# Kernel tuning notes

Hardware: AMD Instinct MI355X
Metric: run time of the kernel (lower is better)

The kernel has to match this reference:

```python
import jax, jax.numpy as jnp
import numpy as np

B, G, IN, F, O = 65536, 6, 512, 256, 18


def setup_inputs() -> dict:
    key = jax.random.key(0)
    ks = jax.random.split(key, 9)
    return {
        "state": jax.random.normal(ks[0], (B, IN), dtype=jnp.float32),
        "action": jax.random.randint(ks[1], (B, 1), 0, O, dtype=jnp.int64),
        "idx": jax.random.randint(ks[2], (B,), 0, G, dtype=jnp.int64),
        # per-game expert Linear weights (stored [in, out] so fwd is x @ W)
        "W1": jax.random.normal(ks[3], (G, IN, F), dtype=jnp.float32) * (1.0 / np.sqrt(IN)),
        "b1": jnp.zeros((G, F), dtype=jnp.float32),
        # shared layer
        "W2": jax.random.normal(ks[4], (F, F), dtype=jnp.float32) * (1.0 / np.sqrt(F)),
        "b2": jnp.zeros((F,), dtype=jnp.float32),
        # per-game Q heads
        "Wq": jax.random.normal(ks[5], (G, F, O), dtype=jnp.float32) * (1.0 / np.sqrt(F)),
        "bq": jnp.zeros((G, O), dtype=jnp.float32),
    }


def reference(state, action, idx, W1, b1, W2, b2, Wq, bq):
    # The torch code processes samples grouped by np.unique(idx) and then
    # torch.cat's the groups: this is a stable sort of samples by idx value.
    perm = jnp.argsort(idx)  # jnp.argsort is stable by default
    sp = state[perm]         # [B, IN], samples in group-sorted order
    ip = idx[perm]           # [B]

    # per-game expert: compute all G tiny linears, select the routed one
    h_all = jax.nn.sigmoid(jnp.einsum('bi,gif->bgf', sp, W1) + b1)  # [B,G,F]
    h1 = jnp.take_along_axis(h_all, ip[:, None, None], axis=1)[:, 0, :]  # [B,F]

    # shared layer ('relu' branch)
    h_f = jax.nn.relu(h1 @ W2 + b2)  # [B,F]

    # stacked per-game heads
    q = jnp.tanh(jnp.einsum('bf,gfo->bgo', h_f, Wq) + bq)  # [B,G,O]

    # action gather: q_acted[b,g] = q[b,g,action[b,0]] (action in ORIGINAL order,
    # exactly as in the torch code, which gathers on the permuted-row q)
    a = jnp.broadcast_to(action[:, :1], (B, G))[..., None]  # [B,G,1]
    q_acted = jnp.take_along_axis(q, a, axis=2)[..., 0]     # [B,G]

    # idx gather (again with idx in ORIGINAL order, matching the torch code)
    q_out = jnp.take_along_axis(q_acted, idx[:, None], axis=1)[:, 0]  # [B]
    return q_out
```

## Files before the change

kernel.cpp:

```cpp
#include <hip/hip_runtime.h>
#include <hip/hip_bf16.h>
#include <math.h>

#define B_N 65536
#define G_N 6
#define IN_N 512
#define F_N 256
#define O_N 18

#define NB 256
#define CHUNK 256

#define TBM 32
#define MAXT (B_N / TBM + G_N)

typedef __bf16 bf16x8 __attribute__((ext_vector_type(8)));
typedef float f32x4 __attribute__((ext_vector_type(4)));

#define WS_BC     0
#define WS_BOFF   8192
#define WS_NTILES 16448
#define WS_DESC   16512
#define WS_W1F    65536
#define WS_W2F    (WS_W1F + 1572864)
#define WS_WQT    (WS_W2F + 131072)
#define WS_PERM   4194304

__device__ __forceinline__ unsigned packcvt(float a, float b) {
    __hip_bfloat162 h = __float22bfloat162_rn(float2{a, b});
    union { __hip_bfloat162 h; unsigned u; } c; c.h = h; return c.u;
}
__device__ __forceinline__ unsigned short f2bf(float f) {
    union { float f; unsigned u; } a; a.f = f;
    unsigned r = a.u + 0x7fffu + ((a.u >> 16) & 1u);
    return (unsigned short)(r >> 16);
}
__device__ __forceinline__ bf16x8 asbf(uint4 u) {
    union { uint4 u; bf16x8 b; } c; c.u = u; return c.b;
}
__device__ __forceinline__ float fast_tanh(float x) {
    float e = __expf(2.0f * x);
    return 1.0f - 2.0f / (e + 1.0f);
}

__global__ void k_hist(const int* __restrict__ idx, int* __restrict__ bc) {
    __shared__ int cnt[G_N];
    int t = threadIdx.x;
    if (t < G_N) cnt[t] = 0;
    __syncthreads();
    int e = blockIdx.x * CHUNK + t;
    atomicAdd(&cnt[idx[e]], 1);
    __syncthreads();
    if (t < G_N) bc[blockIdx.x * G_N + t] = cnt[t];
}

__global__ void k_prefix(const int* __restrict__ bc, int* __restrict__ boff,
                         int* __restrict__ ntiles, int* __restrict__ desc) {
    __shared__ int sbc[NB * G_N];
    __shared__ int tot[G_N], st[G_N];
    __shared__ int tstart[G_N + 1];
    int t = threadIdx.x;
    for (int i = t; i < NB * G_N; i += 256) sbc[i] = bc[i];
    __syncthreads();
    int w = t >> 6, l = t & 63;
    for (int g = w; g < G_N; g += 4) {
        int v[4]; int s = 0;
#pragma unroll
        for (int j = 0; j < 4; j++) { v[j] = sbc[(l * 4 + j) * G_N + g]; s += v[j]; }
        int inc = s;
#pragma unroll
        for (int o = 1; o < 64; o <<= 1) { int x = __shfl_up(inc, o, 64); if (l >= o) inc += x; }
        int run = inc - s;
        if (l == 63) tot[g] = inc;
#pragma unroll
        for (int j = 0; j < 4; j++) { sbc[(l * 4 + j) * G_N + g] = run; run += v[j]; }
    }
    __syncthreads();
    if (t == 0) {
        int acc = 0;
        for (int g = 0; g < G_N; g++) { st[g] = acc; acc += tot[g]; }
        int nt = 0;
        for (int g = 0; g < G_N; g++) { tstart[g] = nt; nt += (tot[g] + TBM - 1) / TBM; }
        tstart[G_N] = nt;
        *ntiles = nt;
    }
    __syncthreads();
    for (int i = t; i < NB * G_N; i += 256) boff[i] = sbc[i] + st[i % G_N];
    int nt = tstart[G_N];
    for (int i = t; i < MAXT; i += 256) {
        int gd = 0, r0 = 0, nr = 0;
        if (i < nt) {
            int g = 0;
            while (g < G_N - 1 && i >= tstart[g + 1]) g++;
            int k = i - tstart[g];
            r0 = st[g] + k * TBM;
            int rem = tot[g] - k * TBM;
            nr = rem < TBM ? rem : TBM;
            gd = g;
        }
        desc[i * 3 + 0] = gd; desc[i * 3 + 1] = r0; desc[i * 3 + 2] = nr;
    }
}

__global__ void k_scatter(const int* __restrict__ idx, const int* __restrict__ boff,
                          int* __restrict__ perm) {
    __shared__ int wcnt[4][G_N];
    __shared__ int base[G_N];
    int t = threadIdx.x, w = t >> 6, l = t & 63;
    int e = blockIdx.x * CHUNK + t;
    int g = idx[e];
    int rank = 0;
    for (int gg = 0; gg < G_N; gg++) {
        unsigned long long m = __ballot(g == gg);
        if (g == gg) rank = __popcll(m & ((1ull << l) - 1ull));
        if (l == 0) wcnt[w][gg] = __popcll(m);
    }
    if (t < G_N) base[t] = boff[blockIdx.x * G_N + t];
    __syncthreads();
    int off = base[g] + rank;
    for (int ww = 0; ww < w; ww++) off += wcnt[ww][g];
    perm[off] = e;
}

__global__ void k_pack_all(const float* __restrict__ W1, const float* __restrict__ W2,
                           const float* __restrict__ Wq,
                           unsigned short* __restrict__ W1f, unsigned short* __restrict__ W2f,
                           float* __restrict__ WqT) {
    int kf = blockIdx.x, w = blockIdx.y, z = blockIdx.z;
    if (z == 6 && kf >= 8) {
        int tid = ((kf - 8) * 8 + w) * 128 + threadIdx.x;
        for (int e = tid; e < G_N * O_N * F_N; e += 8192) {
            int f = e & (F_N - 1);
            int go = e >> 8;
            int g = go / O_N, o = go - g * O_N;
            WqT[e] = Wq[((long)g * F_N + f) * O_N + o];
        }
        return;
    }
    const float* src;
    unsigned short* dst;
    int kfTot;
    if (z < 6) { src = W1 + (long)z * IN_N * F_N; dst = W1f + (long)z * IN_N * F_N; kfTot = 16; }
    else       { src = W2; dst = W2f; kfTot = 8; }
    int f = threadIdx.x >> 6, l = threadIdx.x & 63;
    int lrow = l & 15, q = l >> 4;
    int n = w * 32 + f * 16 + lrow;
    int k0 = kf * 32 + q * 8;
    const float* s = src + (long)k0 * F_N + n;
    unsigned o[4];
#pragma unroll
    for (int j = 0; j < 4; j++)
        o[j] = packcvt(s[(2 * j) * F_N], s[(2 * j + 1) * F_N]);
    unsigned short* d = dst + ((((long)w * kfTot + kf) * 2 + f) * 64 + l) * 8;
    uint4 v = { o[0], o[1], o[2], o[3] };
    *(uint4*)d = v;
}

__global__ __launch_bounds__(512, 6) void k_fused(
    const float* __restrict__ state, const char* __restrict__ w1f,
    const char* __restrict__ w2f, const float* __restrict__ wqt,
    const float* __restrict__ b1, const float* __restrict__ b2,
    const float* __restrict__ bqv,
    const int* __restrict__ action, const int* __restrict__ idx,
    const int* __restrict__ perm, const int* __restrict__ desc,
    float* __restrict__ out) {
    int td = blockIdx.x;
    int g = desc[td * 3 + 0], row0 = desc[td * 3 + 1], nr = desc[td * 3 + 2];
    if (nr == 0) return;

    __shared__ __align__(16) unsigned short smA[TBM * 512];
    __shared__ __align__(16) unsigned short smH[TBM * 256];
    __shared__ float partial[TBM][9];
    __shared__ int gq[TBM], actv[TBM];

    int t = threadIdx.x, w = t >> 6, l = t & 63;
    int lrow = l & 15, q = l >> 4;
    int x0 = lrow & 7;

    const char* B1 = w1f + (((long)g * 8 + w) << 15) + l * 16;
    uint4 nb0 = *(const uint4*)(B1);
    uint4 nb1 = *(const uint4*)(B1 + 1024);

    if (t < TBM) {
        int pos = row0 + t; if (pos > B_N - 1) pos = B_N - 1;
        gq[t] = idx[pos];
        actv[t] = action[pos];
    }

    {
        int m = t >> 4, s = t & 15;
        int pr = row0 + m; if (pr > B_N - 1) pr = B_N - 1;
        const float* src = state + (long)perm[pr] * IN_N + s * 4;
        int cb = s >> 1, h = s & 1, mx = m & 7;
        char* rowbase = (char*)smA + m * 1024 + h * 8;
#pragma unroll
        for (int j = 0; j < 8; j++) {
            float4 v = *(const float4*)(src + j * 64);
            uint2 p = { packcvt(v.x, v.y), packcvt(v.z, v.w) };
            int c = (cb + j * 8) ^ mx;
            *(uint2*)(rowbase + c * 16) = p;
        }
    }
    __syncthreads();

    const char* ar[2];
#pragma unroll
    for (int i = 0; i < 2; i++) ar[i] = (const char*)smA + (i * 16 + lrow) * 1024;

    f32x4 acc[2][2];
#pragma unroll
    for (int i = 0; i < 2; i++)
#pragma unroll
        for (int j = 0; j < 2; j++) acc[i][j] = (f32x4){0.f, 0.f, 0.f, 0.f};

#pragma unroll
    for (int kf = 0; kf < 16; kf++) {
        uint4 cb0 = nb0, cb1 = nb1;
        if (kf < 15) {
            nb0 = *(const uint4*)(B1 + (kf + 1) * 2048);
            nb1 = *(const uint4*)(B1 + (kf + 1) * 2048 + 1024);
        }
        int c = ((kf * 4 + q) ^ x0) * 16;
        bf16x8 af[2];
#pragma unroll
        for (int i = 0; i < 2; i++) af[i] = *(const bf16x8*)(ar[i] + c);
        bf16x8 b0 = asbf(cb0), b1v = asbf(cb1);
#pragma unroll
        for (int i = 0; i < 2; i++) {
            acc[i][0] = __builtin_amdgcn_mfma_f32_16x16x32_bf16(af[i], b0, acc[i][0], 0, 0, 0);
            acc[i][1] = __builtin_amdgcn_mfma_f32_16x16x32_bf16(af[i], b1v, acc[i][1], 0, 0, 0);
        }
    }

    const char* B2 = w2f + ((long)w << 14) + l * 16;
    uint4 m0 = *(const uint4*)(B2);
    uint4 m1 = *(const uint4*)(B2 + 1024);

    {
        int col0 = w * 32 + lrow;
        float bias0 = b1[g * F_N + col0];
        float bias1 = b1[g * F_N + col0 + 16];
        int cc = col0 >> 3, cb2 = (col0 & 7) * 2;
#pragma unroll
        for (int i = 0; i < 2; i++)
#pragma unroll
            for (int r = 0; r < 4; r++) {
                int row = i * 16 + q * 4 + r;
                float v0 = acc[i][0][r] + bias0;
                float v1 = acc[i][1][r] + bias1;
                float sg0 = 1.0f / (1.0f + __expf(-v0));
                float sg1 = 1.0f / (1.0f + __expf(-v1));
                unsigned pk = packcvt(sg0, sg1);
                int rx = row & 7;
                char* base = (char*)smH + row * 512 + cb2;
                *(unsigned short*)(base + ((cc)     ^ rx) * 16) = (unsigned short)pk;
                *(unsigned short*)(base + ((cc + 2) ^ rx) * 16) = (unsigned short)(pk >> 16);
            }
    }
    __syncthreads();

    const char* hr[2];
#pragma unroll
    for (int i = 0; i < 2; i++) hr[i] = (const char*)smH + (i * 16 + lrow) * 512;

    f32x4 acc2[2][2];
#pragma unroll
    for (int i = 0; i < 2; i++)
#pragma unroll
        for (int j = 0; j < 2; j++) acc2[i][j] = (f32x4){0.f, 0.f, 0.f, 0.f};

#pragma unroll
    for (int kf = 0; kf < 8; kf++) {
        uint4 c0 = m0, c1 = m1;
        if (kf < 7) {
            m0 = *(const uint4*)(B2 + (kf + 1) * 2048);
            m1 = *(const uint4*)(B2 + (kf + 1) * 2048 + 1024);
        }
        int c = ((kf * 4 + q) ^ x0) * 16;
        bf16x8 af[2];
#pragma unroll
        for (int i = 0; i < 2; i++) af[i] = *(const bf16x8*)(hr[i] + c);
        bf16x8 b0 = asbf(c0), b1v = asbf(c1);
#pragma unroll
        for (int i = 0; i < 2; i++) {
            acc2[i][0] = __builtin_amdgcn_mfma_f32_16x16x32_bf16(af[i], b0, acc2[i][0], 0, 0, 0);
            acc2[i][1] = __builtin_amdgcn_mfma_f32_16x16x32_bf16(af[i], b1v, acc2[i][1], 0, 0, 0);
        }
    }

    {
        int col0 = w * 32 + lrow;
        float bias0 = b2[col0], bias1 = b2[col0 + 16];
#pragma unroll
        for (int i = 0; i < 2; i++)
#pragma unroll
            for (int r = 0; r < 4; r++) {
                int row = i * 16 + q * 4 + r;
                const float* wp = wqt + ((long)gq[row] * O_N + actv[row]) * F_N;
                float v0 = fmaxf(acc2[i][0][r] + bias0, 0.0f);
                float v1 = fmaxf(acc2[i][1][r] + bias1, 0.0f);
                float s2 = v0 * wp[col0] + v1 * wp[col0 + 16];
                s2 += __shfl_xor(s2, 1, 64);
                s2 += __shfl_xor(s2, 2, 64);
                s2 += __shfl_xor(s2, 4, 64);
                s2 += __shfl_xor(s2, 8, 64);
                if (lrow == 0) partial[row][w] = s2;
            }
    }
    __syncthreads();
    if (t < TBM && t < nr) {
        float s2 = 0.f;
#pragma unroll
        for (int ww = 0; ww < 8; ww++) s2 += partial[t][ww];
        out[row0 + t] = fast_tanh(s2 + bqv[gq[t] * O_N + actv[t]]);
    }
}

extern "C" void kernel_launch(void* const* d_in, const int* in_sizes, int n_in,
                              void* d_out, int out_size, void* d_ws, size_t ws_size,
                              hipStream_t stream) {
    const float* state  = (const float*)d_in[0];
    const int*   action = (const int*)d_in[1];
    const int*   idx    = (const int*)d_in[2];
    const float* W1     = (const float*)d_in[3];
    const float* b1     = (const float*)d_in[4];
    const float* W2     = (const float*)d_in[5];
    const float* b2     = (const float*)d_in[6];
    const float* Wq     = (const float*)d_in[7];
    const float* bq     = (const float*)d_in[8];
    float* out = (float*)d_out;

    char* ws = (char*)d_ws;
    int* bc      = (int*)(ws + WS_BC);
    int* boff    = (int*)(ws + WS_BOFF);
    int* ntiles  = (int*)(ws + WS_NTILES);
    int* desc    = (int*)(ws + WS_DESC);
    unsigned short* W1f = (unsigned short*)(ws + WS_W1F);
    unsigned short* W2f = (unsigned short*)(ws + WS_W2F);
    float* WqT   = (float*)(ws + WS_WQT);
    int* perm    = (int*)(ws + WS_PERM);

    k_hist<<<NB, CHUNK, 0, stream>>>(idx, bc);
    k_prefix<<<1, 256, 0, stream>>>(bc, boff, ntiles, desc);
    k_scatter<<<NB, CHUNK, 0, stream>>>(idx, boff, perm);
    k_pack_all<<<dim3(16, 8, 7), 128, 0, stream>>>(W1, W2, Wq, W1f, W2f, WqT);
    k_fused<<<MAXT, 512, 0, stream>>>(state, (const char*)W1f, (const char*)W2f, WqT,
                                      b1, b2, bq, action, idx, perm, desc, out);
}
```

Measured before the change: 253.4 us.

## Merge all stages into one cooperative persistent kernel with grid syncs

Replaces the five separate launches (histogram, prefix, scatter, weight pack, fused MLP) with a single cooperative kernel that separates the phases with grid.sync(). The main MLP phase becomes a persistent loop over tile descriptors. The aim is to remove per-launch overhead and the inter-kernel gaps. In exchange it adds three grid-wide barriers, runs the prefix scan on one block while the rest wait, and caps the grid at 768 blocks, which may limit how the compute tiles are spread.

```diff
diff --git a/kernel.cpp b/kernel.cpp
--- a/kernel.cpp
+++ b/kernel.cpp
@@ -1,6 +1,9 @@
 #include <hip/hip_runtime.h>
 #include <hip/hip_bf16.h>
+#include <hip/hip_cooperative_groups.h>
 #include <math.h>
+
+namespace cg = cooperative_groups;
 
 #define B_N 65536
 #define G_N 6
@@ -19,7 +22,6 @@
 
 #define WS_BC     0
 #define WS_BOFF   8192
-#define WS_NTILES 16448
 #define WS_DESC   16512
 #define WS_W1F    65536
 #define WS_W2F    (WS_W1F + 1572864)
@@ -30,11 +32,6 @@
     __hip_bfloat162 h = __float22bfloat162_rn(float2{a, b});
     union { __hip_bfloat162 h; unsigned u; } c; c.h = h; return c.u;
 }
-__device__ __forceinline__ unsigned short f2bf(float f) {
-    union { float f; unsigned u; } a; a.f = f;
-    unsigned r = a.u + 0x7fffu + ((a.u >> 16) & 1u);
-    return (unsigned short)(r >> 16);
-}
 __device__ __forceinline__ bf16x8 asbf(uint4 u) {
     union { uint4 u; bf16x8 b; } c; c.u = u; return c.b;
 }
@@ -43,92 +40,12 @@
     return 1.0f - 2.0f / (e + 1.0f);
 }
 
-__global__ void k_hist(const int* __restrict__ idx, int* __restrict__ bc) {
-    __shared__ int cnt[G_N];
-    int t = threadIdx.x;
-    if (t < G_N) cnt[t] = 0;
-    __syncthreads();
-    int e = blockIdx.x * CHUNK + t;
-    atomicAdd(&cnt[idx[e]], 1);
-    __syncthreads();
-    if (t < G_N) bc[blockIdx.x * G_N + t] = cnt[t];
-}
-
-__global__ void k_prefix(const int* __restrict__ bc, int* __restrict__ boff,
-                         int* __restrict__ ntiles, int* __restrict__ desc) {
-    __shared__ int sbc[NB * G_N];
-    __shared__ int tot[G_N], st[G_N];
-    __shared__ int tstart[G_N + 1];
-    int t = threadIdx.x;
-    for (int i = t; i < NB * G_N; i += 256) sbc[i] = bc[i];
-    __syncthreads();
-    int w = t >> 6, l = t & 63;
-    for (int g = w; g < G_N; g += 4) {
-        int v[4]; int s = 0;
-#pragma unroll
-        for (int j = 0; j < 4; j++) { v[j] = sbc[(l * 4 + j) * G_N + g]; s += v[j]; }
-        int inc = s;
-#pragma unroll
-        for (int o = 1; o < 64; o <<= 1) { int x = __shfl_up(inc, o, 64); if (l >= o) inc += x; }
-        int run = inc - s;
-        if (l == 63) tot[g] = inc;
-#pragma unroll
-        for (int j = 0; j < 4; j++) { sbc[(l * 4 + j) * G_N + g] = run; run += v[j]; }
-    }
-    __syncthreads();
-    if (t == 0) {
-        int acc = 0;
-        for (int g = 0; g < G_N; g++) { st[g] = acc; acc += tot[g]; }
-        int nt = 0;
-        for (int g = 0; g < G_N; g++) { tstart[g] = nt; nt += (tot[g] + TBM - 1) / TBM; }
-        tstart[G_N] = nt;
-        *ntiles = nt;
-    }
-    __syncthreads();
-    for (int i = t; i < NB * G_N; i += 256) boff[i] = sbc[i] + st[i % G_N];
-    int nt = tstart[G_N];
-    for (int i = t; i < MAXT; i += 256) {
-        int gd = 0, r0 = 0, nr = 0;
-        if (i < nt) {
-            int g = 0;
-            while (g < G_N - 1 && i >= tstart[g + 1]) g++;
-            int k = i - tstart[g];
-            r0 = st[g] + k * TBM;
-            int rem = tot[g] - k * TBM;
-            nr = rem < TBM ? rem : TBM;
-            gd = g;
-        }
-        desc[i * 3 + 0] = gd; desc[i * 3 + 1] = r0; desc[i * 3 + 2] = nr;
-    }
-}
-
-__global__ void k_scatter(const int* __restrict__ idx, const int* __restrict__ boff,
-                          int* __restrict__ perm) {
-    __shared__ int wcnt[4][G_N];
-    __shared__ int base[G_N];
-    int t = threadIdx.x, w = t >> 6, l = t & 63;
-    int e = blockIdx.x * CHUNK + t;
-    int g = idx[e];
-    int rank = 0;
-    for (int gg = 0; gg < G_N; gg++) {
-        unsigned long long m = __ballot(g == gg);
-        if (g == gg) rank = __popcll(m & ((1ull << l) - 1ull));
-        if (l == 0) wcnt[w][gg] = __popcll(m);
-    }
-    if (t < G_N) base[t] = boff[blockIdx.x * G_N + t];
-    __syncthreads();
-    int off = base[g] + rank;
-    for (int ww = 0; ww < w; ww++) off += wcnt[ww][g];
-    perm[off] = e;
-}
-
-__global__ void k_pack_all(const float* __restrict__ W1, const float* __restrict__ W2,
-                           const float* __restrict__ Wq,
-                           unsigned short* __restrict__ W1f, unsigned short* __restrict__ W2f,
-                           float* __restrict__ WqT) {
-    int kf = blockIdx.x, w = blockIdx.y, z = blockIdx.z;
+__device__ __forceinline__ void pack_unit(int sb, int tl,
+    const float* W1, const float* W2, const float* Wq,
+    unsigned short* W1f, unsigned short* W2f, float* WqT) {
+    int kf = sb & 15, w = (sb >> 4) & 7, z = sb >> 7;
     if (z == 6 && kf >= 8) {
-        int tid = ((kf - 8) * 8 + w) * 128 + threadIdx.x;
+        int tid = ((kf - 8) * 8 + w) * 128 + tl;
         for (int e = tid; e < G_N * O_N * F_N; e += 8192) {
             int f = e & (F_N - 1);
             int go = e >> 8;
@@ -142,7 +59,7 @@
     int kfTot;
     if (z < 6) { src = W1 + (long)z * IN_N * F_N; dst = W1f + (long)z * IN_N * F_N; kfTot = 16; }
     else       { src = W2; dst = W2f; kfTot = 8; }
-    int f = threadIdx.x >> 6, l = threadIdx.x & 63;
+    int f = tl >> 6, l = tl & 63;
     int lrow = l & 15, q = l >> 4;
     int n = w * 32 + f * 16 + lrow;
     int k0 = kf * 32 + q * 8;
@@ -156,163 +73,257 @@
     *(uint4*)d = v;
 }
 
-__global__ __launch_bounds__(512, 6) void k_fused(
-    const float* __restrict__ state, const char* __restrict__ w1f,
-    const char* __restrict__ w2f, const float* __restrict__ wqt,
-    const float* __restrict__ b1, const float* __restrict__ b2,
-    const float* __restrict__ bqv,
-    const int* __restrict__ action, const int* __restrict__ idx,
-    const int* __restrict__ perm, const int* __restrict__ desc,
-    float* __restrict__ out) {
-    int td = blockIdx.x;
-    int g = desc[td * 3 + 0], row0 = desc[td * 3 + 1], nr = desc[td * 3 + 2];
-    if (nr == 0) return;
+__global__ __launch_bounds__(512, 6) void k_mega(
+    const float* state, const int* action, const int* idx,
+    const float* W1, const float* b1, const float* W2, const float* b2,
+    const float* Wq, const float* bqv,
+    int* bc, int* boff, int* desc, int* perm,
+    unsigned short* W1f, unsigned short* W2f, float* WqT,
+    float* out) {
+
+    cg::grid_group grid = cg::this_grid();
+    int bid = blockIdx.x, nb = gridDim.x;
+    int t = threadIdx.x;
 
     __shared__ __align__(16) unsigned short smA[TBM * 512];
     __shared__ __align__(16) unsigned short smH[TBM * 256];
     __shared__ float partial[TBM][9];
     __shared__ int gq[TBM], actv[TBM];
-
-    int t = threadIdx.x, w = t >> 6, l = t & 63;
+    int* scratch = (int*)smA;
+
+    if (bid < NB) {
+        if (t < G_N) scratch[t] = 0;
+        __syncthreads();
+        if (t < CHUNK) atomicAdd(&scratch[idx[bid * CHUNK + t]], 1);
+        __syncthreads();
+        if (t < G_N) bc[bid * G_N + t] = scratch[t];
+    }
+    for (int sb = bid * 4 + (t >> 7); sb < 896; sb += nb * 4)
+        pack_unit(sb, t & 127, W1, W2, Wq, W1f, W2f, WqT);
+    grid.sync();
+
+    if (bid == 0) {
+        int* sbc    = scratch;
+        int* tot    = scratch + NB * G_N;
+        int* stt    = tot + G_N;
+        int* tstart = stt + G_N;
+        for (int i = t; i < NB * G_N; i += 512) sbc[i] = bc[i];
+        __syncthreads();
+        if (t < 256) {
+            int w = t >> 6, l = t & 63;
+            for (int g = w; g < G_N; g += 4) {
+                int v[4]; int s = 0;
+#pragma unroll
+                for (int j = 0; j < 4; j++) { v[j] = sbc[(l * 4 + j) * G_N + g]; s += v[j]; }
+                int inc = s;
+#pragma unroll
+                for (int o = 1; o < 64; o <<= 1) { int x = __shfl_up(inc, o, 64); if (l >= o) inc += x; }
+                int run = inc - s;
+                if (l == 63) tot[g] = inc;
+#pragma unroll
+                for (int j = 0; j < 4; j++) { sbc[(l * 4 + j) * G_N + g] = run; run += v[j]; }
+            }
+        }
+        __syncthreads();
+        if (t == 0) {
+            int acc = 0;
+            for (int g = 0; g < G_N; g++) { stt[g] = acc; acc += tot[g]; }
+            int nt = 0;
+            for (int g = 0; g < G_N; g++) { tstart[g] = nt; nt += (tot[g] + TBM - 1) / TBM; }
+            tstart[G_N] = nt;
+        }
+        __syncthreads();
+        for (int i = t; i < NB * G_N; i += 512) boff[i] = sbc[i] + stt[i % G_N];
+        int nt = tstart[G_N];
+        for (int i = t; i < MAXT; i += 512) {
+            int gd = 0, r0 = 0, nr = 0;
+            if (i < nt) {
+                int g = 0;
+                while (g < G_N - 1 && i >= tstart[g + 1]) g++;
+                int k = i - tstart[g];
+                r0 = stt[g] + k * TBM;
+                int rem = tot[g] - k * TBM;
+                nr = rem < TBM ? rem : TBM;
+                gd = g;
+            }
+            desc[i * 3 + 0] = gd; desc[i * 3 + 1] = r0; desc[i * 3 + 2] = nr;
+        }
+    }
+    grid.sync();
+
+    if (bid < NB) {
+        int* wcnt = scratch;
+        int* base = scratch + 24;
+        bool act = t < CHUNK;
+        int w = t >> 6, l = t & 63;
+        int g = 0, rank = 0;
+        if (act) {
+            g = idx[bid * CHUNK + t];
+            for (int gg2 = 0; gg2 < G_N; gg2++) {
+                unsigned long long m = __ballot(g == gg2);
+                if (g == gg2) rank = __popcll(m & ((1ull << l) - 1ull));
+                if (l == 0) wcnt[w * G_N + gg2] = __popcll(m);
+            }
+        }
+        if (t < G_N) base[t] = boff[bid * G_N + t];
+        __syncthreads();
+        if (act) {
+            int off = base[g] + rank;
+            for (int ww = 0; ww < w; ww++) off += wcnt[ww * G_N + g];
+            perm[off] = bid * CHUNK + t;
+        }
+    }
+    grid.sync();
+
+    const char* w1f = (const char*)W1f;
+    const char* w2f = (const char*)W2f;
+    const float* wqt = WqT;
+
+    int w = t >> 6, l = t & 63;
     int lrow = l & 15, q = l >> 4;
     int x0 = lrow & 7;
 
-    const char* B1 = w1f + (((long)g * 8 + w) << 15) + l * 16;
-    uint4 nb0 = *(const uint4*)(B1);
-    uint4 nb1 = *(const uint4*)(B1 + 1024);
-
-    if (t < TBM) {
-        int pos = row0 + t; if (pos > B_N - 1) pos = B_N - 1;
-        gq[t] = idx[pos];
-        actv[t] = action[pos];
-    }
-
-    {
-        int m = t >> 4, s = t & 15;
-        int pr = row0 + m; if (pr > B_N - 1) pr = B_N - 1;
-        const float* src = state + (long)perm[pr] * IN_N + s * 4;
-        int cb = s >> 1, h = s & 1, mx = m & 7;
-        char* rowbase = (char*)smA + m * 1024 + h * 8;
-#pragma unroll
-        for (int j = 0; j < 8; j++) {
-            float4 v = *(const float4*)(src + j * 64);
-            uint2 p = { packcvt(v.x, v.y), packcvt(v.z, v.w) };
-            int c = (cb + j * 8) ^ mx;
-            *(uint2*)(rowbase + c * 16) = p;
-        }
-    }
-    __syncthreads();
-
-    const char* ar[2];
-#pragma unroll
-    for (int i = 0; i < 2; i++) ar[i] = (const char*)smA + (i * 16 + lrow) * 1024;
-
-    f32x4 acc[2][2];
-#pragma unroll
-    for (int i = 0; i < 2; i++)
-#pragma unroll
-        for (int j = 0; j < 2; j++) acc[i][j] = (f32x4){0.f, 0.f, 0.f, 0.f};
-
-#pragma unroll
-    for (int kf = 0; kf < 16; kf++) {
-        uint4 cb0 = nb0, cb1 = nb1;
-        if (kf < 15) {
-            nb0 = *(const uint4*)(B1 + (kf + 1) * 2048);
-            nb1 = *(const uint4*)(B1 + (kf + 1) * 2048 + 1024);
-        }
-        int c = ((kf * 4 + q) ^ x0) * 16;
-        bf16x8 af[2];
-#pragma unroll
-        for (int i = 0; i < 2; i++) af[i] = *(const bf16x8*)(ar[i] + c);
-        bf16x8 b0 = asbf(cb0), b1v = asbf(cb1);
-#pragma unroll
-        for (int i = 0; i < 2; i++) {
-            acc[i][0] = __builtin_amdgcn_mfma_f32_16x16x32_bf16(af[i], b0, acc[i][0], 0, 0, 0);
-            acc[i][1] = __builtin_amdgcn_mfma_f32_16x16x32_bf16(af[i], b1v, acc[i][1], 0, 0, 0);
-        }
-    }
-
-    const char* B2 = w2f + ((long)w << 14) + l * 16;
-    uint4 m0 = *(const uint4*)(B2);
-    uint4 m1 = *(const uint4*)(B2 + 1024);
-
-    {
-        int col0 = w * 32 + lrow;
-        float bias0 = b1[g * F_N + col0];
-        float bias1 = b1[g * F_N + col0 + 16];
-        int cc = col0 >> 3, cb2 = (col0 & 7) * 2;
+    for (int td = bid; td < MAXT; td += nb) {
+        int g = desc[td * 3 + 0], row0 = desc[td * 3 + 1], nr = desc[td * 3 + 2];
+        if (nr == 0) continue;
+
+        const char* B1 = w1f + (((long)g * 8 + w) << 15) + l * 16;
+        uint4 nb0 = *(const uint4*)(B1);
+        uint4 nb1 = *(const uint4*)(B1 + 1024);
+
+        if (t < TBM) {
+            int pos = row0 + t; if (pos > B_N - 1) pos = B_N - 1;
+            gq[t] = idx[pos];
+            actv[t] = action[pos];
+        }
+
+        {
+            int m = t >> 4, s = t & 15;
+            int pr = row0 + m; if (pr > B_N - 1) pr = B_N - 1;
+            const float* src = state + (long)perm[pr] * IN_N + s * 4;
+            int cb = s >> 1, h = s & 1, mx = m & 7;
+            char* rowbase = (char*)smA + m * 1024 + h * 8;
+#pragma unroll
+            for (int j = 0; j < 8; j++) {
+                float4 v = *(const float4*)(src + j * 64);
+                uint2 p = { packcvt(v.x, v.y), packcvt(v.z, v.w) };
+                int c = (cb + j * 8) ^ mx;
+                *(uint2*)(rowbase + c * 16) = p;
+            }
+        }
+        __syncthreads();
+
+        const char* ar[2];
+#pragma unroll
+        for (int i = 0; i < 2; i++) ar[i] = (const char*)smA + (i * 16 + lrow) * 1024;
+
+        f32x4 acc[2][2];
 #pragma unroll
         for (int i = 0; i < 2; i++)
 #pragma unroll
-            for (int r = 0; r < 4; r++) {
-                int row = i * 16 + q * 4 + r;
-                float v0 = acc[i][0][r] + bias0;
-                float v1 = acc[i][1][r] + bias1;
-                float sg0 = 1.0f / (1.0f + __expf(-v0));
-                float sg1 = 1.0f / (1.0f + __expf(-v1));
-                unsigned pk = packcvt(sg0, sg1);
-                int rx = row & 7;
-                char* base = (char*)smH + row * 512 + cb2;
-                *(unsigned short*)(base + ((cc)     ^ rx) * 16) = (unsigned short)pk;
-                *(unsigned short*)(base + ((cc + 2) ^ rx) * 16) = (unsigned short)(pk >> 16);
-            }
-    }
-    __syncthreads();
-
-    const char* hr[2];
-#pragma unroll
-    for (int i = 0; i < 2; i++) hr[i] = (const char*)smH + (i * 16 + lrow) * 512;
-
-    f32x4 acc2[2][2];
-#pragma unroll
-    for (int i = 0; i < 2; i++)
-#pragma unroll
-        for (int j = 0; j < 2; j++) acc2[i][j] = (f32x4){0.f, 0.f, 0.f, 0.f};
-
-#pragma unroll
-    for (int kf = 0; kf < 8; kf++) {
-        uint4 c0 = m0, c1 = m1;
-        if (kf < 7) {
-            m0 = *(const uint4*)(B2 + (kf + 1) * 2048);
-            m1 = *(const uint4*)(B2 + (kf + 1) * 2048 + 1024);
-        }
-        int c = ((kf * 4 + q) ^ x0) * 16;
-        bf16x8 af[2];
-#pragma unroll
-        for (int i = 0; i < 2; i++) af[i] = *(const bf16x8*)(hr[i] + c);
-        bf16x8 b0 = asbf(c0), b1v = asbf(c1);
-#pragma unroll
-        for (int i = 0; i < 2; i++) {
-            acc2[i][0] = __builtin_amdgcn_mfma_f32_16x16x32_bf16(af[i], b0, acc2[i][0], 0, 0, 0);
-            acc2[i][1] = __builtin_amdgcn_mfma_f32_16x16x32_bf16(af[i], b1v, acc2[i][1], 0, 0, 0);
-        }
-    }
-
-    {
-        int col0 = w * 32 + lrow;
-        float bias0 = b2[col0], bias1 = b2[col0 + 16];
+            for (int j = 0; j < 2; j++) acc[i][j] = (f32x4){0.f, 0.f, 0.f, 0.f};
+
+#pragma unroll
+        for (int kf = 0; kf < 16; kf++) {
+            uint4 cb0 = nb0, cb1 = nb1;
+            if (kf < 15) {
+                nb0 = *(const uint4*)(B1 + (kf + 1) * 2048);
+                nb1 = *(const uint4*)(B1 + (kf + 1) * 2048 + 1024);
+            }
+            int c = ((kf * 4 + q) ^ x0) * 16;
+            bf16x8 af[2];
+#pragma unroll
+            for (int i = 0; i < 2; i++) af[i] = *(const bf16x8*)(ar[i] + c);
+            bf16x8 b0 = asbf(cb0), b1v = asbf(cb1);
+#pragma unroll
+            for (int i = 0; i < 2; i++) {
+                acc[i][0] = __builtin_amdgcn_mfma_f32_16x16x32_bf16(af[i], b0, acc[i][0], 0, 0, 0);
+                acc[i][1] = __builtin_amdgcn_mfma_f32_16x16x32_bf16(af[i], b1v, acc[i][1], 0, 0, 0);
+            }
+        }
+
+        const char* B2 = w2f + ((long)w << 14) + l * 16;
+        uint4 m0 = *(const uint4*)(B2);
+        uint4 m1 = *(const uint4*)(B2 + 1024);
+
+        {
+            int col0 = w * 32 + lrow;
+            float bias0 = b1[g * F_N + col0];
+            float bias1 = b1[g * F_N + col0 + 16];
+            int cc = col0 >> 3, cb2 = (col0 & 7) * 2;
+#pragma unroll
+            for (int i = 0; i < 2; i++)
+#pragma unroll
+                for (int r = 0; r < 4; r++) {
+                    int row = i * 16 + q * 4 + r;
+                    float v0 = acc[i][0][r] + bias0;
+                    float v1 = acc[i][1][r] + bias1;
+                    float sg0 = 1.0f / (1.0f + __expf(-v0));
+                    float sg1 = 1.0f / (1.0f + __expf(-v1));
+                    unsigned pk = packcvt(sg0, sg1);
+                    int rx = row & 7;
+                    char* base = (char*)smH + row * 512 + cb2;
+                    *(unsigned short*)(base + ((cc)     ^ rx) * 16) = (unsigned short)pk;
+                    *(unsigned short*)(base + ((cc + 2) ^ rx) * 16) = (unsigned short)(pk >> 16);
+                }
+        }
+        __syncthreads();
+
+        const char* hr[2];
+#pragma unroll
+        for (int i = 0; i < 2; i++) hr[i] = (const char*)smH + (i * 16 + lrow) * 512;
+
+        f32x4 acc2[2][2];
 #pragma unroll
         for (int i = 0; i < 2; i++)
 #pragma unroll
-            for (int r = 0; r < 4; r++) {
-                int row = i * 16 + q * 4 + r;
-                const float* wp = wqt + ((long)gq[row] * O_N + actv[row]) * F_N;
-                float v0 = fmaxf(acc2[i][0][r] + bias0, 0.0f);
-                float v1 = fmaxf(acc2[i][1][r] + bias1, 0.0f);
-                float s2 = v0 * wp[col0] + v1 * wp[col0 + 16];
-                s2 += __shfl_xor(s2, 1, 64);
-                s2 += __shfl_xor(s2, 2, 64);
-                s2 += __shfl_xor(s2, 4, 64);
-                s2 += __shfl_xor(s2, 8, 64);
-                if (lrow == 0) partial[row][w] = s2;
-            }
-    }
-    __syncthreads();
-    if (t < TBM && t < nr) {
-        float s2 = 0.f;
-#pragma unroll
-        for (int ww = 0; ww < 8; ww++) s2 += partial[t][ww];
-        out[row0 + t] = fast_tanh(s2 + bqv[gq[t] * O_N + actv[t]]);
+            for (int j = 0; j < 2; j++) acc2[i][j] = (f32x4){0.f, 0.f, 0.f, 0.f};
+
+#pragma unroll
+        for (int kf = 0; kf < 8; kf++) {
+            uint4 c0 = m0, c1 = m1;
+            if (kf < 7) {
+                m0 = *(const uint4*)(B2 + (kf + 1) * 2048);
+                m1 = *(const uint4*)(B2 + (kf + 1) * 2048 + 1024);
+            }
+            int c = ((kf * 4 + q) ^ x0) * 16;
+            bf16x8 af[2];
+#pragma unroll
+            for (int i = 0; i < 2; i++) af[i] = *(const bf16x8*)(hr[i] + c);
+            bf16x8 b0 = asbf(c0), b1v = asbf(c1);
+#pragma unroll
+            for (int i = 0; i < 2; i++) {
+                acc2[i][0] = __builtin_amdgcn_mfma_f32_16x16x32_bf16(af[i], b0, acc2[i][0], 0, 0, 0);
+                acc2[i][1] = __builtin_amdgcn_mfma_f32_16x16x32_bf16(af[i], b1v, acc2[i][1], 0, 0, 0);
+            }
+        }
+
+        {
+            int col0 = w * 32 + lrow;
+            float bias0 = b2[col0], bias1 = b2[col0 + 16];
+#pragma unroll
+            for (int i = 0; i < 2; i++)
+#pragma unroll
+                for (int r = 0; r < 4; r++) {
+                    int row = i * 16 + q * 4 + r;
+                    const float* wp = wqt + ((long)gq[row] * O_N + actv[row]) * F_N;
+                    float v0 = fmaxf(acc2[i][0][r] + bias0, 0.0f);
+                    float v1 = fmaxf(acc2[i][1][r] + bias1, 0.0f);
+                    float s2 = v0 * wp[col0] + v1 * wp[col0 + 16];
+                    s2 += __shfl_xor(s2, 1, 64);
+                    s2 += __shfl_xor(s2, 2, 64);
+                    s2 += __shfl_xor(s2, 4, 64);
+                    s2 += __shfl_xor(s2, 8, 64);
+                    if (lrow == 0) partial[row][w] = s2;
+                }
+        }
+        __syncthreads();
+        if (t < TBM && t < nr) {
+            float s2 = 0.f;
+#pragma unroll
+            for (int ww = 0; ww < 8; ww++) s2 += partial[t][ww];
+            out[row0 + t] = fast_tanh(s2 + bqv[gq[t] * O_N + actv[t]]);
+        }
     }
 }
 
@@ -333,17 +344,26 @@
     char* ws = (char*)d_ws;
     int* bc      = (int*)(ws + WS_BC);
     int* boff    = (int*)(ws + WS_BOFF);
-    int* ntiles  = (int*)(ws + WS_NTILES);
     int* desc    = (int*)(ws + WS_DESC);
     unsigned short* W1f = (unsigned short*)(ws + WS_W1F);
     unsigned short* W2f = (unsigned short*)(ws + WS_W2F);
     float* WqT   = (float*)(ws + WS_WQT);
     int* perm    = (int*)(ws + WS_PERM);
 
-    k_hist<<<NB, CHUNK, 0, stream>>>(idx, bc);
-    k_prefix<<<1, 256, 0, stream>>>(bc, boff, ntiles, desc);
-    k_scatter<<<NB, CHUNK, 0, stream>>>(idx, boff, perm);
-    k_pack_all<<<dim3(16, 8, 7), 128, 0, stream>>>(W1, W2, Wq, W1f, W2f, WqT);
-    k_fused<<<MAXT, 512, 0, stream>>>(state, (const char*)W1f, (const char*)W2f, WqT,
-                                      b1, b2, bq, action, idx, perm, desc, out);
-}
+    int maxb = 0;
+    if (hipOccupancyMaxActiveBlocksPerMultiprocessor(&maxb, k_mega, 512, 0) != hipSuccess || maxb < 1)
+        maxb = 1;
+    int grid = maxb * 256;
+    if (grid > 768) grid = 768;
+    if (grid < NB)  grid = NB;
+
+    void* args[] = {
+        (void*)&state, (void*)&action, (void*)&idx,
+        (void*)&W1, (void*)&b1, (void*)&W2, (void*)&b2,
+        (void*)&Wq, (void*)&bq,
+        (void*)&bc, (void*)&boff, (void*)&desc, (void*)&perm,
+        (void*)&W1f, (void*)&W2f, (void*)&WqT,
+        (void*)&out
+    };
+    hipLaunchCooperativeKernel((const void*)k_mega, dim3(grid), dim3(512), args, 0, stream);
+}
```

New measurement: 500.4 us. 97.5% more time.
